# Performance work log

Hardware: AMD Instinct MI355X
Metric: run time of the kernel (lower is better)

Reference implementation:

```python
import jax, jax.numpy as jnp
import numpy as np

# dims: batch, time points, control channels (input_path_dim+1), cde state, mlp width
B, T, C, S, H = 64, 256, 16, 64, 128

# Tsit5 explicit tableau (5th-order solution weights; FSAL 7th stage has b7=0 and is skipped)
A21 = 0.161
A31, A32 = -0.008480655492356989, 0.335480655492357
A41, A42, A43 = 2.8971530571054935, -6.359448489975075, 4.3622954328695815
A51, A52, A53, A54 = 5.325864828439257, -11.748883564062828, 7.4955393428898365, -0.09249506636175525
A61, A62, A63, A64, A65 = 5.86145544294642, -12.92096931784711, 8.159367898576159, -0.071584973281401, -0.028269050394068383
C2, C3, C4, C5 = 0.161, 0.327, 0.9, 0.9800255409045097
BW = (0.09646076681806523, 0.01, 0.4798896504144996, 1.379008574103742, -3.290069515436081, 2.324710524099774)


def _mlp(x, ws, bs, final_act):
    for w, b in zip(ws[:-1], bs[:-1]):
        x = jax.nn.softplus(x @ w.T + b)
    return final_act(x @ ws[-1].T + bs[-1])


def _from_6d(v):  # (..., 6) -> (..., 3, 3) via Gram-Schmidt (Zhou et al. 6D rotation rep)
    a1, a2 = v[..., :3], v[..., 3:]
    b1 = a1 / jnp.linalg.norm(a1, axis=-1, keepdims=True)
    a2p = a2 - jnp.sum(b1 * a2, axis=-1, keepdims=True) * b1
    b2 = a2p / jnp.linalg.norm(a2p, axis=-1, keepdims=True)
    b3 = jnp.cross(b1, b2)
    return jnp.stack([b1, b2, b3], axis=-1)


def setup_inputs() -> dict:
    key = jax.random.key(0)
    ks = jax.random.split(key, 8)

    def lin(k, fan_in, fan_out):  # equinox Linear init: U(-1/sqrt(in), 1/sqrt(in))
        k1, k2 = jax.random.split(k)
        lim = 1.0 / np.sqrt(fan_in)
        w = jax.random.uniform(k1, (fan_out, fan_in), minval=-lim, maxval=lim, dtype=jnp.float32)
        b = jax.random.uniform(k2, (fan_out,), minval=-lim, maxval=lim, dtype=jnp.float32)
        return w, b

    ic_w0, ic_b0 = lin(ks[0], C, H)
    ic_w1, ic_b1 = lin(ks[1], H, H)
    ic_w2, ic_b2 = lin(ks[2], H, S)
    vf_w0, vf_b0 = lin(ks[3], S, H)
    vf_w1, vf_b1 = lin(ks[4], H, H)
    vf_w2, vf_b2 = lin(ks[5], H, S * C)
    ro_w, ro_b = lin(ks[6], S, 6)
    control_values = jax.random.normal(ks[7], (B, T, C), dtype=jnp.float32)
    return dict(control_values=control_values,
                ic_w0=ic_w0, ic_b0=ic_b0, ic_w1=ic_w1, ic_b1=ic_b1, ic_w2=ic_w2, ic_b2=ic_b2,
                vf_w0=vf_w0, vf_b0=vf_b0, vf_w1=vf_w1, vf_b1=vf_b1, vf_w2=vf_w2, vf_b2=vf_b2,
                ro_w=ro_w, ro_b=ro_b)


def reference(control_values, ic_w0, ic_b0, ic_w1, ic_b1, ic_w2, ic_b2,
              vf_w0, vf_b0, vf_w1, vf_b1, vf_w2, vf_b2, ro_w, ro_b):
    b, t, c = control_values.shape
    s = ic_w2.shape[0]
    h = 1.0 / (t - 1)  # uniform ts = linspace(0, 1, T)
    xs = control_values
    # backward-Hermite derivatives: d[i] = (x[i]-x[i-1])/h, d[0] = d[1]
    d = jnp.diff(xs, axis=1) / h                       # (B, T-1, C)
    dfull = jnp.concatenate([d[:, :1], d], axis=1)     # (B, T, C)

    ic_ws, ic_bs = [ic_w0, ic_w1, ic_w2], [ic_b0, ic_b1, ic_b2]
    vf_ws, vf_bs = [vf_w0, vf_w1, vf_w2], [vf_b0, vf_b1, vf_b2]

    y0 = _mlp(xs[:, 0], ic_ws, ic_bs, lambda x: x)     # (B, S)

    def vf_mat(y):  # (B, S) -> (B, S, C)
        return _mlp(y, vf_ws, vf_bs, jnp.tanh).reshape(b, s, c)

    def step(y, iv):
        yi, yip1, di, dip1 = iv  # each (B, C): interval endpoints & Hermite derivs

        def dXdt(sc):  # derivative of cubic Hermite at local coord sc in [0,1]
            s2 = sc * sc
            return (((6 * s2 - 6 * sc) / h) * yi + (3 * s2 - 4 * sc + 1) * di
                    + ((6 * sc - 6 * s2) / h) * yip1 + (3 * s2 - 2 * sc) * dip1)

        def f(yy, sc):
            return jnp.einsum('bsc,bc->bs', vf_mat(yy), dXdt(sc))

        k1 = f(y, 0.0)
        k2 = f(y + h * (A21 * k1), C2)
        k3 = f(y + h * (A31 * k1 + A32 * k2), C3)
        k4 = f(y + h * (A41 * k1 + A42 * k2 + A43 * k3), C4)
        k5 = f(y + h * (A51 * k1 + A52 * k2 + A53 * k3 + A54 * k4), C5)
        k6 = f(y + h * (A61 * k1 + A62 * k2 + A63 * k3 + A64 * k4 + A65 * k5), 1.0)
        yn = y + h * (BW[0] * k1 + BW[1] * k2 + BW[2] * k3 + BW[3] * k4 + BW[4] * k5 + BW[5] * k6)
        return yn, yn

    ivs = (jnp.swapaxes(xs[:, :-1], 0, 1), jnp.swapaxes(xs[:, 1:], 0, 1),
           jnp.swapaxes(dfull[:, :-1], 0, 1), jnp.swapaxes(dfull[:, 1:], 0, 1))
    _, ys = jax.lax.scan(step, y0, ivs)                # (T-1, B, S)
    hidden = jnp.swapaxes(jnp.concatenate([y0[None], ys], axis=0), 0, 1)  # (B, T, S)

    out6 = hidden @ ro_w.T + ro_b                      # (B, T, 6); identity readout activation
    return _from_6d(out6)                              # (B, T, 3, 3)
```

## Files before the change

### kernel.cpp

```cpp
#include <hip/hip_runtime.h>


typedef float float4v __attribute__((ext_vector_type(4)));
typedef float float2v __attribute__((ext_vector_type(2)));

__device__ __forceinline__ float dot4(float4v a, float4v b) {
  return a.x * b.x + a.y * b.y + a.z * b.z + a.w * b.w;
}

__device__ __forceinline__ float softplus_fast(float x) {
  float z = __expf(-fabsf(x));
  return fmaxf(x, 0.f) + __logf(1.f + z);
}

__device__ __forceinline__ float tanh_hw(float x) {
  float e = __expf(2.f * x);
  return 1.f - 2.f * __builtin_amdgcn_rcpf(e + 1.f);
}

__global__ __attribute__((amdgpu_waves_per_eu(2, 2)))
__launch_bounds__(512, 1) void cde_main(
    const float* __restrict__ xs,
    const float* __restrict__ icw0, const float* __restrict__ icb0,
    const float* __restrict__ icw1, const float* __restrict__ icb1,
    const float* __restrict__ icw2, const float* __restrict__ icb2,
    const float* __restrict__ vfw0, const float* __restrict__ vfb0,
    const float* __restrict__ vfw1, const float* __restrict__ vfb1,
    const float* __restrict__ vfw2, const float* __restrict__ vfb2,
    float* __restrict__ ybuf) {
  constexpr float Ac[6][5] = {
      {0.f, 0.f, 0.f, 0.f, 0.f},
      {0.161f, 0.f, 0.f, 0.f, 0.f},
      {-0.008480655492356989f, 0.335480655492357f, 0.f, 0.f, 0.f},
      {2.8971530571054935f, -6.359448489975075f, 4.3622954328695815f, 0.f, 0.f},
      {5.325864828439257f, -11.748883564062828f, 7.4955393428898365f,
       -0.09249506636175525f, 0.f},
      {5.86145544294642f, -12.92096931784711f, 8.159367898576159f,
       -0.071584973281401f, -0.028269050394068383f}};
  constexpr float SCv[6] = {0.f, 0.161f, 0.327f, 0.9f, 0.9800255409045097f, 1.f};
  constexpr float BWv[6] = {0.09646076681806523f, 0.01f, 0.4798896504144996f,
                            1.379008574103742f, -3.290069515436081f,
                            2.324710524099774f};

  const int tid = threadIdx.x;
  const int w = tid >> 6, l = tid & 63;
  const int b = blockIdx.x;

  __shared__ float sW2t[38][1024];
  __shared__ __align__(16) float sYtw[8][64];
  __shared__ __align__(16) float sH1[128];
  __shared__ __align__(16) float sH2[128];
  __shared__ float sK[6][64];

  for (int i = tid; i < 38 * 1024; i += 512) {
    int k = i >> 10, r = i & 1023;
    sW2t[k][r] = vfw2[(size_t)r * 128 + 90 + k];
  }

  const int r0 = tid * 2, r1 = r0 + 1;
  float w2a[72], w2b[72];
  {
    const float4v* p0 = (const float4v*)(vfw2 + (size_t)r0 * 128);
    const float4v* p1 = (const float4v*)(vfw2 + (size_t)r1 * 128);
#pragma unroll
    for (int kk = 0; kk < 18; ++kk) {
      float4v a = p0[kk], c = p1[kk];
      w2a[4 * kk + 0] = a.x; w2a[4 * kk + 1] = a.y;
      w2a[4 * kk + 2] = a.z; w2a[4 * kk + 3] = a.w;
      w2b[4 * kk + 0] = c.x; w2b[4 * kk + 1] = c.y;
      w2b[4 * kk + 2] = c.z; w2b[4 * kk + 3] = c.w;
    }
  }
#pragma unroll
  for (int kk = 0; kk < 72; ++kk)
    asm volatile("" : "+v"(w2a[kk]), "+v"(w2b[kk]));

  const int ii = tid >> 2, q4 = tid & 3;
  float w0r[16], w1r[32];
  {
    const float4v* p = (const float4v*)(vfw0 + (size_t)ii * 64 + q4 * 16);
#pragma unroll
    for (int kk = 0; kk < 4; ++kk) {
      float4v a = p[kk];
      w0r[4 * kk] = a.x; w0r[4 * kk + 1] = a.y;
      w0r[4 * kk + 2] = a.z; w0r[4 * kk + 3] = a.w;
    }
  }
  {
    const float4v* p = (const float4v*)(vfw1 + (size_t)ii * 128 + q4 * 32);
#pragma unroll
    for (int kk = 0; kk < 8; ++kk) {
      float4v a = p[kk];
      w1r[4 * kk] = a.x; w1r[4 * kk + 1] = a.y;
      w1r[4 * kk + 2] = a.z; w1r[4 * kk + 3] = a.w;
    }
  }
#pragma unroll
  for (int kk = 0; kk < 16; ++kk) asm volatile("" : "+v"(w0r[kk]));
#pragma unroll
  for (int kk = 0; kk < 32; ++kk) asm volatile("" : "+v"(w1r[kk]));

  const float b2r0 = vfb2[r0], b2r1 = vfb2[r1];
  const int c0 = (2 * l) & 15;
  const float b0i = vfb0[ii], b1i = vfb1[ii];

  const float* Xb = xs + (size_t)b * 4096;
  float* yb = ybuf + (size_t)b * 16384;

  __syncthreads();

  float* sTA = &sK[0][0];
  float* sTB = sH1;
  if (tid < 128) {
    float a = icb0[tid];
    const float* wr = icw0 + tid * 16;
#pragma unroll
    for (int k = 0; k < 16; ++k) a += wr[k] * Xb[k];
    sTA[tid] = softplus_fast(a);
  }
  __syncthreads();
  if (tid < 128) {
    float a = icb1[tid];
    const float* wr = icw1 + tid * 128;
    for (int k = 0; k < 128; ++k) a += wr[k] * sTA[k];
    sTB[tid] = softplus_fast(a);
  }
  __syncthreads();
  if (tid < 64) {
    float a = icb2[tid];
    const float* wr = icw2 + tid * 128;
    for (int k = 0; k < 128; ++k) a += wr[k] * sTB[k];
    sH2[tid] = a;
  }
  __syncthreads();
  float yreg = sH2[l];
  if (w == 0) yb[l] = yreg;

  const float hstep = 1.f / 255.f;
  const float invh = 255.f;

#pragma unroll 1
  for (int t = 0; t < 255; ++t) {
    float2v xt = *(const float2v*)(Xb + t * 16 + c0);
    float2v xt1 = *(const float2v*)(Xb + (t + 1) * 16 + c0);
    float2v xtm = xt;
    if (t != 0) xtm = *(const float2v*)(Xb + (t - 1) * 16 + c0);
    const float u0 = xt.x - xt1.x, u1 = xt.y - xt1.y;
    const float dp0 = (xt1.x - xt.x) * invh;
    const float dp1 = (xt1.y - xt.y) * invh;
    float di0 = (t == 0) ? dp0 : (xt.x - xtm.x) * invh;
    float di1 = (t == 0) ? dp1 : (xt.y - xtm.y) * invh;
#pragma unroll 1
    for (int j = 0; j < 6; ++j) {
      const float* wr0 = vfw2 + (size_t)r0 * 128;
      const float* wr1 = vfw2 + (size_t)r1 * 128;
      float4v sa0 = *(const float4v*)(wr0 + 72);
      float4v sa1 = *(const float4v*)(wr0 + 76);
      float4v sa2 = *(const float4v*)(wr0 + 80);
      float4v sa3 = *(const float4v*)(wr0 + 84);
      float2v sa4 = *(const float2v*)(wr0 + 88);
      float4v sb0 = *(const float4v*)(wr1 + 72);
      float4v sb1 = *(const float4v*)(wr1 + 76);
      float4v sb2 = *(const float4v*)(wr1 + 80);
      float4v sb3 = *(const float4v*)(wr1 + 84);
      float2v sb4 = *(const float2v*)(wr1 + 88);
      {
        float yt = yreg;
#pragma unroll
        for (int m = 0; m < 5; ++m)
          if (m < j) yt += hstep * Ac[j][m] * sK[m][l];
        sYtw[w][l] = yt;
      }
      asm volatile("s_waitcnt lgkmcnt(0)" ::: "memory");
      const float sc = SCv[j], s2 = sc * sc;
      const float a1 = (6.f * s2 - 6.f * sc) * invh;
      const float a2 = 3.f * s2 - 4.f * sc + 1.f;
      const float a3 = 3.f * s2 - 2.f * sc;
      const float dx0 = a1 * u0 + a2 * di0 + a3 * dp0;
      const float dx1 = a1 * u1 + a2 * di1 + a3 * dp1;
      {
        const float4v* yv = (const float4v*)(&sYtw[w][0] + q4 * 16);
        float4v y0 = yv[0], y1 = yv[1], y2 = yv[2], y3 = yv[3];
        float s = w0r[0] * y0.x + w0r[1] * y0.y + w0r[2] * y0.z +
                  w0r[3] * y0.w + w0r[4] * y1.x + w0r[5] * y1.y +
                  w0r[6] * y1.z + w0r[7] * y1.w + w0r[8] * y2.x +
                  w0r[9] * y2.y + w0r[10] * y2.z + w0r[11] * y2.w +
                  w0r[12] * y3.x + w0r[13] * y3.y + w0r[14] * y3.z +
                  w0r[15] * y3.w;
        s += __shfl_xor(s, 1);
        s += __shfl_xor(s, 2);
        if (q4 == 0) sH1[ii] = softplus_fast(s + b0i);
      }
      __syncthreads();
      {
        const float4v* hv = (const float4v*)(sH1 + q4 * 32);
        float s = 0.f;
#pragma unroll
        for (int kk = 0; kk < 8; ++kk) {
          float4v h = hv[kk];
          s += w1r[4 * kk] * h.x + w1r[4 * kk + 1] * h.y +
               w1r[4 * kk + 2] * h.z + w1r[4 * kk + 3] * h.w;
        }
        s += __shfl_xor(s, 1);
        s += __shfl_xor(s, 2);
        if (q4 == 0) sH2[ii] = softplus_fast(s + b1i);
      }
      __syncthreads();
      {
        const float4v* hv = (const float4v*)sH2;
        float s0 = 0.f, s1 = 0.f;
#pragma unroll
        for (int kk = 0; kk < 18; ++kk) {
          float4v h = hv[kk];
          s0 += w2a[4 * kk] * h.x + w2a[4 * kk + 1] * h.y +
                w2a[4 * kk + 2] * h.z + w2a[4 * kk + 3] * h.w;
          s1 += w2b[4 * kk] * h.x + w2b[4 * kk + 1] * h.y +
                w2b[4 * kk + 2] * h.z + w2b[4 * kk + 3] * h.w;
        }
        {
          float4v h0 = hv[18], h1 = hv[19], h2 = hv[20], h3 = hv[21];
          float2v h4 = *(const float2v*)(sH2 + 88);
          s0 += dot4(sa0, h0) + dot4(sa1, h1) + dot4(sa2, h2) +
                dot4(sa3, h3) + sa4.x * h4.x + sa4.y * h4.y;
          s1 += dot4(sb0, h0) + dot4(sb1, h1) + dot4(sb2, h2) +
                dot4(sb3, h3) + sb4.x * h4.x + sb4.y * h4.y;
        }
#pragma unroll 4
        for (int k2 = 0; k2 < 19; ++k2) {
          float2v hk = *(const float2v*)(sH2 + 90 + 2 * k2);
          float2v wlo = *(const float2v*)&sW2t[2 * k2][r0];
          float2v whi = *(const float2v*)&sW2t[2 * k2 + 1][r0];
          s0 += wlo.x * hk.x + whi.x * hk.y;
          s1 += wlo.y * hk.x + whi.y * hk.y;
        }
        float f = tanh_hw(s0 + b2r0) * dx0 + tanh_hw(s1 + b2r1) * dx1;
        f += __shfl_xor(f, 1);
        f += __shfl_xor(f, 2);
        f += __shfl_xor(f, 4);
        if ((tid & 7) == 0) sK[j][tid >> 3] = f;
      }
      __syncthreads();
    }
    {
      float yn = yreg;
#pragma unroll
      for (int m = 0; m < 6; ++m) yn += hstep * BWv[m] * sK[m][l];
      yreg = yn;
      if (w == 0) yb[(size_t)(t + 1) * 64 + l] = yn;
    }
  }
}

__global__ __launch_bounds__(256) void readout(
    const float* __restrict__ ybuf, const float* __restrict__ row,
    const float* __restrict__ rob, float* __restrict__ out) {
  int idx = blockIdx.x * blockDim.x + threadIdx.x;
  const float* y = ybuf + (size_t)idx * 64;
  float p[6];
#pragma unroll
  for (int o = 0; o < 6; ++o) {
    const float4v* rr = (const float4v*)(row + o * 64);
    const float4v* yv = (const float4v*)y;
    float s = 0.f;
#pragma unroll
    for (int k = 0; k < 16; ++k) s += dot4(rr[k], yv[k]);
    p[o] = s + rob[o];
  }
  float a1x = p[0], a1y = p[1], a1z = p[2];
  float a2x = p[3], a2y = p[4], a2z = p[5];
  float n1 = rsqrtf(a1x * a1x + a1y * a1y + a1z * a1z);
  float b1x = a1x * n1, b1y = a1y * n1, b1z = a1z * n1;
  float d = b1x * a2x + b1y * a2y + b1z * a2z;
  float px = a2x - d * b1x, py = a2y - d * b1y, pz = a2z - d * b1z;
  float n2 = rsqrtf(px * px + py * py + pz * pz);
  float b2x = px * n2, b2y = py * n2, b2z = pz * n2;
  float b3x = b1y * b2z - b1z * b2y;
  float b3y = b1z * b2x - b1x * b2z;
  float b3z = b1x * b2y - b1y * b2x;
  float* o = out + (size_t)idx * 9;
  o[0] = b1x; o[1] = b2x; o[2] = b3x;
  o[3] = b1y; o[4] = b2y; o[5] = b3y;
  o[6] = b1z; o[7] = b2z; o[8] = b3z;
}

extern "C" void kernel_launch(void* const* d_in, const int* in_sizes, int n_in,
                              void* d_out, int out_size, void* d_ws,
                              size_t ws_size, hipStream_t stream) {
  (void)in_sizes; (void)n_in; (void)out_size; (void)ws_size;
  const float* xs   = (const float*)d_in[0];
  const float* icw0 = (const float*)d_in[1];
  const float* icb0 = (const float*)d_in[2];
  const float* icw1 = (const float*)d_in[3];
  const float* icb1 = (const float*)d_in[4];
  const float* icw2 = (const float*)d_in[5];
  const float* icb2 = (const float*)d_in[6];
  const float* vfw0 = (const float*)d_in[7];
  const float* vfb0 = (const float*)d_in[8];
  const float* vfw1 = (const float*)d_in[9];
  const float* vfb1 = (const float*)d_in[10];
  const float* vfw2 = (const float*)d_in[11];
  const float* vfb2 = (const float*)d_in[12];
  const float* row  = (const float*)d_in[13];
  const float* rob  = (const float*)d_in[14];
  float* ybuf = (float*)d_ws;

  hipLaunchKernelGGL(cde_main, dim3(64), dim3(512), 0, stream,
                     xs, icw0, icb0, icw1, icb1, icw2, icb2,
                     vfw0, vfb0, vfw1, vfb1, vfw2, vfb2, ybuf);
  hipLaunchKernelGGL(readout, dim3(64), dim3(256), 0, stream,
                     ybuf, row, rob, (float*)d_out);
}
```

Baseline: 6.524 ms.

## Hold full W2 rows in AccVGPRs and move W0/W1 to padded LDS

Each thread's two full 128-wide rows of the third vector-field layer weight now sit in accumulation registers, written with v_accvgpr_write and read back with v_accvgpr_read. This removes the per-stage global reloads of columns 72-89 and the LDS-transposed tail of W2. The first two layer weights move from registers into padded shared memory to free VGPRs, and the W2 dot product is split into four accumulators for more instruction-level parallelism. In exchange, every stage adds 256 accvgpr reads per thread and LDS reads for W0 and W1. The volatile inline asm may also limit how the compiler schedules instructions.

```diff
diff --git a/kernel.cpp b/kernel.cpp
--- a/kernel.cpp
+++ b/kernel.cpp
@@ -17,6 +17,11 @@
   float e = __expf(2.f * x);
   return 1.f - 2.f * __builtin_amdgcn_rcpf(e + 1.f);
 }
+
+#define AWRITE(dst, src) \
+  asm volatile("v_accvgpr_write_b32 %0, %1" : "=a"(dst) : "v"(src))
+#define AREAD(dst, src) \
+  asm volatile("v_accvgpr_read_b32 %0, %1" : "=v"(dst) : "a"(src))
 
 __global__ __attribute__((amdgpu_waves_per_eu(2, 2)))
 __launch_bounds__(512, 1) void cde_main(
@@ -46,62 +51,40 @@
   const int w = tid >> 6, l = tid & 63;
   const int b = blockIdx.x;
 
-  __shared__ float sW2t[38][1024];
+  __shared__ float sW0[128 * 68];
+  __shared__ float sW1[128 * 132];
   __shared__ __align__(16) float sYtw[8][64];
   __shared__ __align__(16) float sH1[128];
   __shared__ __align__(16) float sH2[128];
   __shared__ float sK[6][64];
 
-  for (int i = tid; i < 38 * 1024; i += 512) {
-    int k = i >> 10, r = i & 1023;
-    sW2t[k][r] = vfw2[(size_t)r * 128 + 90 + k];
-  }
+  for (int i = tid; i < 8192; i += 512) sW0[(i >> 6) * 68 + (i & 63)] = vfw0[i];
+  for (int i = tid; i < 16384; i += 512)
+    sW1[(i >> 7) * 132 + (i & 127)] = vfw1[i];
 
   const int r0 = tid * 2, r1 = r0 + 1;
-  float w2a[72], w2b[72];
+  float w2r0[128], w2r1[128];
   {
     const float4v* p0 = (const float4v*)(vfw2 + (size_t)r0 * 128);
     const float4v* p1 = (const float4v*)(vfw2 + (size_t)r1 * 128);
 #pragma unroll
-    for (int kk = 0; kk < 18; ++kk) {
-      float4v a = p0[kk], c = p1[kk];
-      w2a[4 * kk + 0] = a.x; w2a[4 * kk + 1] = a.y;
-      w2a[4 * kk + 2] = a.z; w2a[4 * kk + 3] = a.w;
-      w2b[4 * kk + 0] = c.x; w2b[4 * kk + 1] = c.y;
-      w2b[4 * kk + 2] = c.z; w2b[4 * kk + 3] = c.w;
+    for (int c4 = 0; c4 < 32; ++c4) {
+      float4v a = p0[c4], c = p1[c4];
+      w2r0[4 * c4 + 0] = a.x; w2r0[4 * c4 + 1] = a.y;
+      w2r0[4 * c4 + 2] = a.z; w2r0[4 * c4 + 3] = a.w;
+      w2r1[4 * c4 + 0] = c.x; w2r1[4 * c4 + 1] = c.y;
+      w2r1[4 * c4 + 2] = c.z; w2r1[4 * c4 + 3] = c.w;
     }
   }
 #pragma unroll
-  for (int kk = 0; kk < 72; ++kk)
-    asm volatile("" : "+v"(w2a[kk]), "+v"(w2b[kk]));
-
-  const int ii = tid >> 2, q4 = tid & 3;
-  float w0r[16], w1r[32];
-  {
-    const float4v* p = (const float4v*)(vfw0 + (size_t)ii * 64 + q4 * 16);
-#pragma unroll
-    for (int kk = 0; kk < 4; ++kk) {
-      float4v a = p[kk];
-      w0r[4 * kk] = a.x; w0r[4 * kk + 1] = a.y;
-      w0r[4 * kk + 2] = a.z; w0r[4 * kk + 3] = a.w;
-    }
-  }
-  {
-    const float4v* p = (const float4v*)(vfw1 + (size_t)ii * 128 + q4 * 32);
-#pragma unroll
-    for (int kk = 0; kk < 8; ++kk) {
-      float4v a = p[kk];
-      w1r[4 * kk] = a.x; w1r[4 * kk + 1] = a.y;
-      w1r[4 * kk + 2] = a.z; w1r[4 * kk + 3] = a.w;
-    }
-  }
-#pragma unroll
-  for (int kk = 0; kk < 16; ++kk) asm volatile("" : "+v"(w0r[kk]));
-#pragma unroll
-  for (int kk = 0; kk < 32; ++kk) asm volatile("" : "+v"(w1r[kk]));
+  for (int c = 0; c < 128; ++c) {
+    AWRITE(w2r0[c], w2r0[c]);
+    AWRITE(w2r1[c], w2r1[c]);
+  }
 
   const float b2r0 = vfb2[r0], b2r1 = vfb2[r1];
   const int c0 = (2 * l) & 15;
+  const int ii = tid >> 2, q4 = tid & 3;
   const float b0i = vfb0[ii], b1i = vfb1[ii];
 
   const float* Xb = xs + (size_t)b * 4096;
@@ -152,18 +135,6 @@
     float di1 = (t == 0) ? dp1 : (xt.y - xtm.y) * invh;
 #pragma unroll 1
     for (int j = 0; j < 6; ++j) {
-      const float* wr0 = vfw2 + (size_t)r0 * 128;
-      const float* wr1 = vfw2 + (size_t)r1 * 128;
-      float4v sa0 = *(const float4v*)(wr0 + 72);
-      float4v sa1 = *(const float4v*)(wr0 + 76);
-      float4v sa2 = *(const float4v*)(wr0 + 80);
-      float4v sa3 = *(const float4v*)(wr0 + 84);
-      float2v sa4 = *(const float2v*)(wr0 + 88);
-      float4v sb0 = *(const float4v*)(wr1 + 72);
-      float4v sb1 = *(const float4v*)(wr1 + 76);
-      float4v sb2 = *(const float4v*)(wr1 + 80);
-      float4v sb3 = *(const float4v*)(wr1 + 84);
-      float2v sb4 = *(const float2v*)(wr1 + 88);
       {
         float yt = yreg;
 #pragma unroll
@@ -179,28 +150,21 @@
       const float dx0 = a1 * u0 + a2 * di0 + a3 * dp0;
       const float dx1 = a1 * u1 + a2 * di1 + a3 * dp1;
       {
+        const float4v* wr = (const float4v*)(sW0 + ii * 68 + q4 * 16);
         const float4v* yv = (const float4v*)(&sYtw[w][0] + q4 * 16);
-        float4v y0 = yv[0], y1 = yv[1], y2 = yv[2], y3 = yv[3];
-        float s = w0r[0] * y0.x + w0r[1] * y0.y + w0r[2] * y0.z +
-                  w0r[3] * y0.w + w0r[4] * y1.x + w0r[5] * y1.y +
-                  w0r[6] * y1.z + w0r[7] * y1.w + w0r[8] * y2.x +
-                  w0r[9] * y2.y + w0r[10] * y2.z + w0r[11] * y2.w +
-                  w0r[12] * y3.x + w0r[13] * y3.y + w0r[14] * y3.z +
-                  w0r[15] * y3.w;
+        float s = dot4(wr[0], yv[0]) + dot4(wr[1], yv[1]) +
+                  dot4(wr[2], yv[2]) + dot4(wr[3], yv[3]);
         s += __shfl_xor(s, 1);
         s += __shfl_xor(s, 2);
         if (q4 == 0) sH1[ii] = softplus_fast(s + b0i);
       }
       __syncthreads();
       {
+        const float4v* wr = (const float4v*)(sW1 + ii * 132 + q4 * 32);
         const float4v* hv = (const float4v*)(sH1 + q4 * 32);
         float s = 0.f;
 #pragma unroll
-        for (int kk = 0; kk < 8; ++kk) {
-          float4v h = hv[kk];
-          s += w1r[4 * kk] * h.x + w1r[4 * kk + 1] * h.y +
-               w1r[4 * kk + 2] * h.z + w1r[4 * kk + 3] * h.w;
-        }
+        for (int kk = 0; kk < 8; ++kk) s += dot4(wr[kk], hv[kk]);
         s += __shfl_xor(s, 1);
         s += __shfl_xor(s, 2);
         if (q4 == 0) sH2[ii] = softplus_fast(s + b1i);
@@ -208,31 +172,25 @@
       __syncthreads();
       {
         const float4v* hv = (const float4v*)sH2;
-        float s0 = 0.f, s1 = 0.f;
-#pragma unroll
-        for (int kk = 0; kk < 18; ++kk) {
-          float4v h = hv[kk];
-          s0 += w2a[4 * kk] * h.x + w2a[4 * kk + 1] * h.y +
-                w2a[4 * kk + 2] * h.z + w2a[4 * kk + 3] * h.w;
-          s1 += w2b[4 * kk] * h.x + w2b[4 * kk + 1] * h.y +
-                w2b[4 * kk + 2] * h.z + w2b[4 * kk + 3] * h.w;
+        float s0a = 0.f, s0b = 0.f, s1a = 0.f, s1b = 0.f;
+#pragma unroll
+        for (int c4 = 0; c4 < 32; ++c4) {
+          float4v hk = hv[c4];
+          float wa0, wa1, wa2, wa3, wb0, wb1, wb2, wb3;
+          AREAD(wa0, w2r0[4 * c4 + 0]);
+          AREAD(wa1, w2r0[4 * c4 + 1]);
+          AREAD(wa2, w2r0[4 * c4 + 2]);
+          AREAD(wa3, w2r0[4 * c4 + 3]);
+          AREAD(wb0, w2r1[4 * c4 + 0]);
+          AREAD(wb1, w2r1[4 * c4 + 1]);
+          AREAD(wb2, w2r1[4 * c4 + 2]);
+          AREAD(wb3, w2r1[4 * c4 + 3]);
+          s0a += wa0 * hk.x + wa2 * hk.z;
+          s0b += wa1 * hk.y + wa3 * hk.w;
+          s1a += wb0 * hk.x + wb2 * hk.z;
+          s1b += wb1 * hk.y + wb3 * hk.w;
         }
-        {
-          float4v h0 = hv[18], h1 = hv[19], h2 = hv[20], h3 = hv[21];
-          float2v h4 = *(const float2v*)(sH2 + 88);
-          s0 += dot4(sa0, h0) + dot4(sa1, h1) + dot4(sa2, h2) +
-                dot4(sa3, h3) + sa4.x * h4.x + sa4.y * h4.y;
-          s1 += dot4(sb0, h0) + dot4(sb1, h1) + dot4(sb2, h2) +
-                dot4(sb3, h3) + sb4.x * h4.x + sb4.y * h4.y;
-        }
-#pragma unroll 4
-        for (int k2 = 0; k2 < 19; ++k2) {
-          float2v hk = *(const float2v*)(sH2 + 90 + 2 * k2);
-          float2v wlo = *(const float2v*)&sW2t[2 * k2][r0];
-          float2v whi = *(const float2v*)&sW2t[2 * k2 + 1][r0];
-          s0 += wlo.x * hk.x + whi.x * hk.y;
-          s1 += wlo.y * hk.x + whi.y * hk.y;
-        }
+        float s0 = s0a + s0b, s1 = s1a + s1b;
         float f = tanh_hw(s0 + b2r0) * dx0 + tanh_hw(s1 + b2r1) * dx1;
         f += __shfl_xor(f, 1);
         f += __shfl_xor(f, 2);
```

Result: slower. 13.38 ms (+105.0%).
